# Optimization experiments

Measured on AMD Instinct MI355X. Metric: run time of the kernel, lower is better.

The kernel has to match this reference:

```python
import jax, jax.numpy as jnp
import numpy as np

B, S, D = 8, 2048, 768
SCALE = jnp.sqrt(jnp.float32(D))


def setup_inputs() -> dict:
    key = jax.random.key(0)
    ks = jax.random.split(key, 9)
    sd = 1.0 / np.sqrt(D)
    return {
        "x": jax.random.normal(ks[0], (B, S, D), jnp.float32),
        "Wq": jax.random.normal(ks[1], (D, D), jnp.float32) * sd,
        "bq": jax.random.normal(ks[2], (D,), jnp.float32) * sd,
        "Wk": jax.random.normal(ks[3], (D, D), jnp.float32) * sd,
        "bk": jax.random.normal(ks[4], (D,), jnp.float32) * sd,
        "Wv": jax.random.normal(ks[5], (D, D), jnp.float32) * sd,
        "bv": jax.random.normal(ks[6], (D,), jnp.float32) * sd,
        "Wp": jax.random.normal(ks[7], (D, D), jnp.float32) * sd,
        "bp": jax.random.normal(ks[8], (D,), jnp.float32) * sd,
    }


def reference(x, Wq, bq, Wk, bk, Wv, bv, Wp, bp):
    # Linear layers: y = x @ W^T + b (torch nn.Linear convention)
    Q = jnp.einsum("bsd,ed->bse", x, Wq) + bq
    K = jnp.einsum("bsd,ed->bse", x, Wk) + bk
    V = jnp.einsum("bsd,ed->bse", x, Wv) + bv
    # Full attention matrix (no head split in original module)
    alpha = jnp.einsum("bqd,bkd->bqk", Q, K) / SCALE  # [B,S,S]
    alpha = jax.nn.softmax(alpha, axis=-1)
    # dropout is identity in eval mode
    out = jnp.einsum("bqk,bkd->bqd", alpha, V)
    out = jnp.einsum("bsd,ed->bse", out, Wp) + bp
    return out
```

## Files before the change

### kernel.cpp

```cpp
#include <hip/hip_runtime.h>
#include <stdint.h>


typedef __attribute__((ext_vector_type(8))) short short8;
typedef __attribute__((ext_vector_type(4))) float f32x4;

typedef const __attribute__((address_space(1))) void gvoid_t;
typedef __attribute__((address_space(3))) void lvoid_t;

__device__ __forceinline__ float b2f(unsigned short u) {
  union { unsigned int u; float f; } v;
  v.u = ((unsigned int)u) << 16;
  return v.f;
}
__device__ __forceinline__ unsigned short f2b(float f) {
  union { float f; unsigned int u; } v; v.f = f;
  unsigned int u = v.u;
  return (unsigned short)((u + 0x7fffu + ((u >> 16) & 1u)) >> 16);
}

struct Cvt9 {
  const void* s[9];
  unsigned short* d[9];
  long long n8[9];
  long long total8;
};

__global__ __launch_bounds__(256) void convert_inputs(Cvt9 C) {
  long long g = (long long)blockIdx.x * 256 + threadIdx.x;
  if (g >= C.total8) return;
  int s = 0;
  long long off = g;
  while (off >= C.n8[s]) { off -= C.n8[s]; ++s; }
  const float* sf = (const float*)C.s[s] + off * 8;
  unsigned short* dp = C.d[s] + off * 8;
  float4 a = ((const float4*)sf)[0];
  float4 b = ((const float4*)sf)[1];
  uint4 o;
  o.x = (unsigned int)f2b(a.x) | ((unsigned int)f2b(a.y) << 16);
  o.y = (unsigned int)f2b(a.z) | ((unsigned int)f2b(a.w) << 16);
  o.z = (unsigned int)f2b(b.x) | ((unsigned int)f2b(b.y) << 16);
  o.w = (unsigned int)f2b(b.z) | ((unsigned int)f2b(b.w) << 16);
  *(uint4*)dp = o;
}

template<int NQ>
__device__ __forceinline__ void gemm256(
    const unsigned short* __restrict__ Ag,
    const unsigned short* __restrict__ Bg,
    const int lda, const int ldb, const int NT,
    unsigned short* lds, f32x4 (&acc)[8][NQ])
{
  const int t    = threadIdx.x;
  const int w    = t >> 6;
  const int lane = t & 63;
  const int lo   = lane & 15;
  const int quad = lane >> 4;
  const int wr   = w >> 2;
  const int wcn  = w & 3;
  const int swz  = ((t & 7) ^ ((t >> 3) & 7)) << 3;
  const int wslot = w * 512;
  constexpr int SBUF_B = (4 + NQ) * 8192;
  constexpr int SBUF_S = SBUF_B / 2;

  const unsigned lbase = (unsigned)(uintptr_t)(void*)lds;
  const unsigned sb0 = (unsigned)((quad ^ (lo & 7)) << 4);
  const unsigned sb1 = (unsigned)(((4 + quad) ^ (lo & 7)) << 4);
  const unsigned aA0 = lbase + wr * 16384 + lo * 128 + sb0;
  const unsigned aA1 = lbase + wr * 16384 + lo * 128 + sb1;
  const unsigned bB  = lbase + 32768u + (unsigned)(wcn * 16 * NQ + lo) * 128;
  const unsigned aB0 = bB + sb0;
  const unsigned aB1 = bB + sb1;

  short8 af[4][2], bf0[2][2], bf1[2][2];

#define STG(gb, ld, kt, q, reg)                                                   \
  __builtin_amdgcn_global_load_lds(                                               \
      (gvoid_t*)((gb) + (size_t)((q) * 64 + (t >> 3)) * (ld) + (kt) * 64 + swz),  \
      (lvoid_t*)((reg) + wslot), 16, 0, 0)
#define SA02(kt) { unsigned short* r_ = lds + ((kt) & 1) * SBUF_S;         \
                   STG(Ag, lda, (kt), 0, r_); STG(Ag, lda, (kt), 2, r_ + 8192); }
#define SA13(kt) { unsigned short* r_ = lds + ((kt) & 1) * SBUF_S;         \
                   STG(Ag, lda, (kt), 1, r_ + 4096); STG(Ag, lda, (kt), 3, r_ + 12288); }
#define SBALL(kt) { unsigned short* r_ = lds + ((kt) & 1) * SBUF_S + 16384; \
                    STG(Bg, ldb, (kt), 0, r_); STG(Bg, ldb, (kt), 1, r_ + 4096); \
                    STG(Bg, ldb, (kt), 2, r_ + 8192); \
                    if constexpr (NQ == 4) STG(Bg, ldb, (kt), 3, r_ + 12288); }
#define DSR(d, a, IMM) asm volatile("ds_read_b128 %0, %1 offset:" #IMM : "=v"(d) : "v"(a))
#define RDA(MH, bo) {                                                 \
  const unsigned a0_ = aA0 + (bo) + (MH) * 8192;                      \
  const unsigned a1_ = aA1 + (bo) + (MH) * 8192;                      \
  DSR(af[0][0], a0_, 0);    DSR(af[0][1], a1_, 0);                    \
  DSR(af[1][0], a0_, 2048); DSR(af[1][1], a1_, 2048);                 \
  DSR(af[2][0], a0_, 4096); DSR(af[2][1], a1_, 4096);                 \
  DSR(af[3][0], a0_, 6144); DSR(af[3][1], a1_, 6144); }
#define RDB(BF, NB, NFR, bo) {                                        \
  const unsigned b0_ = aB0 + (bo) + (NB) * 2048;                      \
  const unsigned b1_ = aB1 + (bo) + (NB) * 2048;                      \
  DSR(BF[0][0], b0_, 0);    DSR(BF[0][1], b1_, 0);                    \
  if ((NFR) == 2) { DSR(BF[1][0], b0_, 2048); DSR(BF[1][1], b1_, 2048); } }
#define MMA(MH, NB, BF, NFR) {                                                \
  __builtin_amdgcn_s_barrier();                                               \
  asm volatile("s_waitcnt lgkmcnt(0)" ::: "memory");                          \
  __builtin_amdgcn_sched_barrier(0);                                          \
  __builtin_amdgcn_s_setprio(1);                                              \
  _Pragma("unroll") for (int kc = 0; kc < 2; ++kc)                            \
  _Pragma("unroll") for (int mi = 0; mi < 4; ++mi)                            \
  _Pragma("unroll") for (int ni = 0; ni < (NFR); ++ni)                        \
    acc[(MH)*4 + mi][(NB) + ni] = __builtin_amdgcn_mfma_f32_16x16x32_bf16(    \
        af[mi][kc], BF[ni][kc], acc[(MH)*4 + mi][(NB) + ni], 0, 0, 0);        \
  __builtin_amdgcn_s_setprio(0);                                              \
  __builtin_amdgcn_sched_barrier(0);                                          \
  __builtin_amdgcn_s_barrier(); }
#define VMS() { if constexpr (NQ == 4) asm volatile("s_waitcnt vmcnt(8)" ::: "memory"); \
                else                   asm volatile("s_waitcnt vmcnt(7)" ::: "memory"); }
#define VM0() asm volatile("s_waitcnt vmcnt(0)" ::: "memory")

  SA02(0); SBALL(0); SA13(0);
  SA02(1); SBALL(1); SA13(1);
  VMS();
  __builtin_amdgcn_s_barrier();

  for (int kt = 0; kt < NT - 2; ++kt) {
    const unsigned bo = (unsigned)((kt & 1) * SBUF_B);
    RDA(0, bo); RDB(bf0, 0, 2, bo);                       MMA(0, 0, bf0, 2);
    RDB(bf1, 2, NQ - 2, bo); SA02(kt + 2);                MMA(0, 2, bf1, NQ - 2);
    RDA(1, bo); SBALL(kt + 2);                            MMA(1, 0, bf0, 2);
    SA13(kt + 2); VMS();                                  MMA(1, 2, bf1, NQ - 2);
  }
  {
    const unsigned bo = (unsigned)((NT & 1) * SBUF_B);
    RDA(0, bo); RDB(bf0, 0, 2, bo);                       MMA(0, 0, bf0, 2);
    RDB(bf1, 2, NQ - 2, bo);                              MMA(0, 2, bf1, NQ - 2);
    RDA(1, bo);                                           MMA(1, 0, bf0, 2);
    VM0();                                                MMA(1, 2, bf1, NQ - 2);
  }
  {
    const unsigned bo = (unsigned)(((NT - 1) & 1) * SBUF_B);
    RDA(0, bo); RDB(bf0, 0, 2, bo);                       MMA(0, 0, bf0, 2);
    RDB(bf1, 2, NQ - 2, bo);                              MMA(0, 2, bf1, NQ - 2);
    RDA(1, bo);                                           MMA(1, 0, bf0, 2);
                                                          MMA(1, 2, bf1, NQ - 2);
  }
#undef STG
#undef SA02
#undef SA13
#undef SBALL
#undef DSR
#undef RDA
#undef RDB
#undef MMA
#undef VMS
#undef VM0
}

template<int MODE, int NQ>
__device__ __forceinline__ void epi_bf16(
    unsigned short* Ls, f32x4 (&acc)[8][NQ], int h,
    const unsigned short* bias_n0, const float* rlbase, float scale,
    unsigned short* Cg, int ldc)
{
  constexpr int RS = 64 * NQ + 8;
  const int t = threadIdx.x, w = t >> 6, lane = t & 63;
  const int lo = lane & 15, quad = lane >> 4, wr = w >> 2, wcn = w & 3;
  __syncthreads();
  if (wr == h) {
    float bvv[NQ];
    if (MODE == 0) {
#pragma unroll
      for (int nf = 0; nf < NQ; ++nf) bvv[nf] = b2f(bias_n0[wcn * 16 * NQ + nf * 16 + lo]);
    }
#pragma unroll
    for (int mf = 0; mf < 8; ++mf) {
      const int r0 = mf * 16 + quad * 4;
      float rv[4];
      if (MODE == 3) {
#pragma unroll
        for (int r = 0; r < 4; ++r) rv[r] = __builtin_amdgcn_rcpf(rlbase[h * 128 + r0 + r]);
      }
#pragma unroll
      for (int nf = 0; nf < NQ; ++nf) {
        const int col = wcn * 16 * NQ + nf * 16 + lo;
#pragma unroll
        for (int r = 0; r < 4; ++r) {
          float v = acc[mf][nf][r];
          if (MODE == 0)      v += bvv[nf];
          else if (MODE == 2) v = __expf(fminf(v * scale, 30.f));
          else if (MODE == 3) v *= rv[r];
          Ls[(r0 + r) * RS + col] = f2b(v);
        }
      }
    }
  }
  __syncthreads();
#pragma unroll
  for (int u0 = 0; u0 < 2 * NQ; ++u0) {
    const int u = u0 * 512 + t, row = u / (8 * NQ), c16 = (u % (8 * NQ)) * 8;
    *(uint4*)(Cg + (size_t)(h * 128 + row) * ldc + c16) = *(const uint4*)(Ls + row * RS + c16);
  }
}

__global__ __launch_bounds__(512, 2) void qkv_k(
    const unsigned short* __restrict__ xb,
    const unsigned short* __restrict__ Wq, const unsigned short* __restrict__ bq,
    const unsigned short* __restrict__ Wk, const unsigned short* __restrict__ bk,
    const unsigned short* __restrict__ Wv, const unsigned short* __restrict__ bv,
    unsigned short* __restrict__ qb, unsigned short* __restrict__ kb,
    unsigned short* __restrict__ vt)
{
  __shared__ unsigned short smem[57344];
  const int sel = blockIdx.y >> 2;
  const int n0  = (blockIdx.y & 3) * 192;
  const int m0  = blockIdx.x * 256;

  const unsigned short* W;
  const unsigned short* bi;
  if (sel == 0)      { W = Wq; bi = bq; }
  else if (sel == 1) { W = Wk; bi = bk; }
  else               { W = Wv; bi = bv; }

  f32x4 acc[8][3] = {};
  gemm256<3>(xb + (size_t)m0 * 768, W + (size_t)n0 * 768, 768, 768, 12, smem, acc);

  if (sel < 2) {
    unsigned short* dst = (sel == 0 ? qb : kb) + (size_t)m0 * 768 + n0;
    epi_bf16<0, 3>(smem, acc, 0, bi + n0, nullptr, 0.f, dst, 768);
    epi_bf16<0, 3>(smem, acc, 1, bi + n0, nullptr, 0.f, dst, 768);
    return;
  }

  const int t = threadIdx.x, w = t >> 6, lane = t & 63;
  const int lo = lane & 15, quad = lane >> 4, wr = w >> 2, wcn = w & 3;
  const int bb2 = m0 >> 11, sin = m0 & 2047;
  unsigned short* Ls = smem;
#pragma unroll
  for (int ec = 0; ec < 3; ++ec) {
    __syncthreads();
#pragma unroll
    for (int nf = 0; nf < 3; ++nf) {
      const int ebase = wcn * 48 + nf * 16;
      if ((ebase >> 6) == ec) {
        const float bvv = b2f(bi[n0 + ebase + lo]);
#pragma unroll
        for (int mf = 0; mf < 8; ++mf) {
          const int srow = wr * 128 + mf * 16 + quad * 4;
          ushort4 pk;
          pk.x = f2b(acc[mf][nf][0] + bvv);
          pk.y = f2b(acc[mf][nf][1] + bvv);
          pk.z = f2b(acc[mf][nf][2] + bvv);
          pk.w = f2b(acc[mf][nf][3] + bvv);
          *(ushort4*)(Ls + ((ebase & 63) + lo) * 264 + srow) = pk;
        }
      }
    }
    __syncthreads();
    unsigned short* Vb = vt + (size_t)bb2 * 1572864 + (size_t)(n0 + ec * 64) * 2048 + sin;
#pragma unroll
    for (int u0 = 0; u0 < 4; ++u0) {
      const int u = u0 * 512 + t, e = u >> 5, s16 = (u & 31) * 8;
      *(uint4*)(Vb + (size_t)e * 2048 + s16) = *(const uint4*)(Ls + e * 264 + s16);
    }
  }
}

__global__ __launch_bounds__(512, 2) void score_k(
    const unsigned short* __restrict__ Q, const unsigned short* __restrict__ Kb,
    unsigned short* __restrict__ E, float* __restrict__ rl, float scale)
{
  __shared__ unsigned short smem[65536];
  const int m0 = blockIdx.x * 256, n0 = blockIdx.y * 256, bz = blockIdx.z;

  f32x4 acc[8][4] = {};
  gemm256<4>(Q + (size_t)bz * 1572864 + (size_t)m0 * 768,
             Kb + (size_t)bz * 1572864 + (size_t)n0 * 768, 768, 768, 12, smem, acc);

  const int t = threadIdx.x;
  unsigned short* Eg = E + (size_t)bz * 4194304 + (size_t)m0 * 2048 + n0;
#pragma unroll
  for (int h = 0; h < 2; ++h) {
    epi_bf16<2, 4>(smem, acc, h, nullptr, nullptr, scale, Eg, 2048);
    const int row = t >> 2, seg = t & 3;
    const unsigned short* lr = smem + row * 264 + seg * 64;
    float s = 0.f;
#pragma unroll
    for (int q8 = 0; q8 < 8; ++q8) {
      const int qq = ((q8 + row) & 7) * 8;
      uint4 v = *(const uint4*)(lr + qq);
      unsigned int uu[4] = {v.x, v.y, v.z, v.w};
#pragma unroll
      for (int c = 0; c < 4; ++c)
        s += b2f((unsigned short)(uu[c] & 0xffffu)) + b2f((unsigned short)(uu[c] >> 16));
    }
    s += __shfl_xor(s, 1);
    s += __shfl_xor(s, 2);
    if (seg == 0) atomicAdd(rl + bz * 2048 + m0 + h * 128 + row, s);
  }
}

__global__ __launch_bounds__(512, 2) void pv_k(
    const unsigned short* __restrict__ E, const unsigned short* __restrict__ Vt,
    const float* __restrict__ rl, unsigned short* __restrict__ attn)
{
  __shared__ unsigned short smem[57344];
  const int m0 = blockIdx.x * 256, n0 = blockIdx.y * 192, bz = blockIdx.z;

  f32x4 acc[8][3] = {};
  gemm256<3>(E + (size_t)bz * 4194304 + (size_t)m0 * 2048,
             Vt + (size_t)bz * 1572864 + (size_t)n0 * 2048, 2048, 2048, 32, smem, acc);

  const float* rlb = rl + bz * 2048 + m0;
  unsigned short* Cg = attn + (size_t)bz * 1572864 + (size_t)m0 * 768 + n0;
  epi_bf16<3, 3>(smem, acc, 0, nullptr, rlb, 0.f, Cg, 768);
  epi_bf16<3, 3>(smem, acc, 1, nullptr, rlb, 0.f, Cg, 768);
}

__global__ __launch_bounds__(512, 2) void out_k(
    const unsigned short* __restrict__ attn,
    const unsigned short* __restrict__ Wp, const unsigned short* __restrict__ bp,
    float* __restrict__ Of)
{
  __shared__ unsigned short smem[57344];
  const int m0 = blockIdx.x * 256, n0 = blockIdx.y * 192;

  f32x4 acc[8][3] = {};
  gemm256<3>(attn + (size_t)m0 * 768, Wp + (size_t)n0 * 768, 768, 768, 12, smem, acc);

  const int t = threadIdx.x, w = t >> 6, lane = t & 63;
  const int lo = lane & 15, quad = lane >> 4, wr = w >> 2, wcn = w & 3;
  float* Lf = (float*)smem;
#pragma unroll
  for (int p = 0; p < 4; ++p) {
    __syncthreads();
    if (wr == (p >> 1)) {
#pragma unroll
      for (int mi = 0; mi < 4; ++mi) {
        const int mf = (p & 1) * 4 + mi;
        const int r0 = mi * 16 + quad * 4;
#pragma unroll
        for (int nf = 0; nf < 3; ++nf) {
          const int col = wcn * 48 + nf * 16 + lo;
          const float bvv = b2f(bp[n0 + col]);
#pragma unroll
          for (int r = 0; r < 4; ++r)
            Lf[(r0 + r) * 196 + col] = acc[mf][nf][r] + bvv;
        }
      }
    }
    __syncthreads();
#pragma unroll
    for (int u0 = 0; u0 < 6; ++u0) {
      const int u = u0 * 512 + t, row = u / 48, c4 = (u % 48) * 4;
      *(float4*)(Of + (size_t)(m0 + p * 64 + row) * 768 + n0 + c4) =
          *(const float4*)(Lf + row * 196 + c4);
    }
  }
}

extern "C" void kernel_launch(void* const* d_in, const int* in_sizes, int n_in,
                              void* d_out, int out_size, void* d_ws, size_t ws_size,
                              hipStream_t stream) {
  (void)in_sizes; (void)n_in; (void)out_size; (void)ws_size;

  char* ws = (char*)d_ws;
  float* rl    = (float*)(ws + 4096);
  unsigned short* wcv = (unsigned short*)(ws + ((size_t)1 << 20));
  unsigned short* qb  = (unsigned short*)(ws + ((size_t)8  << 20));
  unsigned short* kb  = (unsigned short*)(ws + ((size_t)32 << 20));
  unsigned short* vt  = (unsigned short*)(ws + ((size_t)56 << 20));
  unsigned short* eb  = (unsigned short*)(ws + ((size_t)80 << 20));
  unsigned short* xb  = eb;
  unsigned short* attn = qb;

  unsigned short* wqb = wcv;
  unsigned short* bqb = wcv + 589824;
  unsigned short* wkb = wcv + 590592;
  unsigned short* bkb = wcv + 1180416;
  unsigned short* wvb = wcv + 1181184;
  unsigned short* bvb = wcv + 1771008;
  unsigned short* wpb = wcv + 1771776;
  unsigned short* bpb = wcv + 2361600;

  const float inv_scale = 0.036084391824351615f;

  Cvt9 cv;
  cv.s[0] = d_in[0]; cv.d[0] = xb;  cv.n8[0] = 12582912 / 8;
  cv.s[1] = d_in[1]; cv.d[1] = wqb; cv.n8[1] = 589824 / 8;
  cv.s[2] = d_in[2]; cv.d[2] = bqb; cv.n8[2] = 768 / 8;
  cv.s[3] = d_in[3]; cv.d[3] = wkb; cv.n8[3] = 589824 / 8;
  cv.s[4] = d_in[4]; cv.d[4] = bkb; cv.n8[4] = 768 / 8;
  cv.s[5] = d_in[5]; cv.d[5] = wvb; cv.n8[5] = 589824 / 8;
  cv.s[6] = d_in[6]; cv.d[6] = bvb; cv.n8[6] = 768 / 8;
  cv.s[7] = d_in[7]; cv.d[7] = wpb; cv.n8[7] = 589824 / 8;
  cv.s[8] = d_in[8]; cv.d[8] = bpb; cv.n8[8] = 768 / 8;
  cv.total8 = (12582912 + 4 * (589824 + 768)) / 8;
  convert_inputs<<<(unsigned)((cv.total8 + 255) / 256), dim3(256), 0, stream>>>(cv);

  hipMemsetAsync(rl, 0, 16384 * sizeof(float), stream);

  qkv_k<<<dim3(64, 12, 1), dim3(512), 0, stream>>>(xb, wqb, bqb, wkb, bkb, wvb, bvb, qb, kb, vt);

  score_k<<<dim3(8, 8, 8), dim3(512), 0, stream>>>(qb, kb, eb, rl, inv_scale);

  pv_k<<<dim3(8, 4, 8), dim3(512), 0, stream>>>(eb, vt, rl, attn);

  out_k<<<dim3(64, 4, 1), dim3(512), 0, stream>>>(attn, wpb, bpb, (float*)d_out);
}
```

Baseline: 321.0 us.

## Halve GEMM M-tile to 128 rows and double grid sizes across all kernels

Replaces the 256-row block GEMM with a 128-row variant that uses fewer accumulators, less LDS and a simplified two-phase MMA pipeline. Grids are doubled in M and launch bounds are raised to four blocks per SM. Epilogues are simplified to a single pass. The aim is more blocks for better CU occupancy and wave coverage on the small grids, at the cost of less operand reuse per block and more global traffic for the B operand.

After: 337.4 us. 1.05x slower.

```diff
diff --git a/kernel.cpp b/kernel.cpp
--- a/kernel.cpp
+++ b/kernel.cpp
@@ -45,11 +45,11 @@
 }
 
 template<int NQ>
-__device__ __forceinline__ void gemm256(
+__device__ __forceinline__ void gemm128(
     const unsigned short* __restrict__ Ag,
     const unsigned short* __restrict__ Bg,
     const int lda, const int ldb, const int NT,
-    unsigned short* lds, f32x4 (&acc)[8][NQ])
+    unsigned short* lds, f32x4 (&acc)[4][NQ])
 {
   const int t    = threadIdx.x;
   const int w    = t >> 6;
@@ -60,103 +60,93 @@
   const int wcn  = w & 3;
   const int swz  = ((t & 7) ^ ((t >> 3) & 7)) << 3;
   const int wslot = w * 512;
-  constexpr int SBUF_B = (4 + NQ) * 8192;
+  constexpr int SBUF_B = (2 + NQ) * 8192;
   constexpr int SBUF_S = SBUF_B / 2;
 
   const unsigned lbase = (unsigned)(uintptr_t)(void*)lds;
   const unsigned sb0 = (unsigned)((quad ^ (lo & 7)) << 4);
   const unsigned sb1 = (unsigned)(((4 + quad) ^ (lo & 7)) << 4);
-  const unsigned aA0 = lbase + wr * 16384 + lo * 128 + sb0;
-  const unsigned aA1 = lbase + wr * 16384 + lo * 128 + sb1;
-  const unsigned bB  = lbase + 32768u + (unsigned)(wcn * 16 * NQ + lo) * 128;
-  const unsigned aB0 = bB + sb0;
-  const unsigned aB1 = bB + sb1;
-
-  short8 af[4][2], bf0[2][2], bf1[2][2];
-
-#define STG(gb, ld, kt, q, reg)                                                   \
+  const unsigned aA0 = lbase + (unsigned)(wr * 64 + lo) * 128 + sb0;
+  const unsigned aA1 = lbase + (unsigned)(wr * 64 + lo) * 128 + sb1;
+  const unsigned aB0 = lbase + 16384u + (unsigned)(wcn * 16 * NQ + lo) * 128 + sb0;
+  const unsigned aB1 = lbase + 16384u + (unsigned)(wcn * 16 * NQ + lo) * 128 + sb1;
+
+  short8 af[4][2], bf[NQ][2];
+
+#define STG(gb, ld, kt, q, soff)                                                  \
   __builtin_amdgcn_global_load_lds(                                               \
       (gvoid_t*)((gb) + (size_t)((q) * 64 + (t >> 3)) * (ld) + (kt) * 64 + swz),  \
-      (lvoid_t*)((reg) + wslot), 16, 0, 0)
-#define SA02(kt) { unsigned short* r_ = lds + ((kt) & 1) * SBUF_S;         \
-                   STG(Ag, lda, (kt), 0, r_); STG(Ag, lda, (kt), 2, r_ + 8192); }
-#define SA13(kt) { unsigned short* r_ = lds + ((kt) & 1) * SBUF_S;         \
-                   STG(Ag, lda, (kt), 1, r_ + 4096); STG(Ag, lda, (kt), 3, r_ + 12288); }
-#define SBALL(kt) { unsigned short* r_ = lds + ((kt) & 1) * SBUF_S + 16384; \
-                    STG(Bg, ldb, (kt), 0, r_); STG(Bg, ldb, (kt), 1, r_ + 4096); \
-                    STG(Bg, ldb, (kt), 2, r_ + 8192); \
-                    if constexpr (NQ == 4) STG(Bg, ldb, (kt), 3, r_ + 12288); }
+      (lvoid_t*)(lds + ((kt) & 1) * SBUF_S + (soff) + wslot), 16, 0, 0)
+#define SALL(kt) { STG(Ag, lda, (kt), 0, 0); STG(Ag, lda, (kt), 1, 4096);      \
+                   STG(Bg, ldb, (kt), 0, 8192); STG(Bg, ldb, (kt), 1, 12288);  \
+                   STG(Bg, ldb, (kt), 2, 16384);                               \
+                   if constexpr (NQ == 4) STG(Bg, ldb, (kt), 3, 20480); }
 #define DSR(d, a, IMM) asm volatile("ds_read_b128 %0, %1 offset:" #IMM : "=v"(d) : "v"(a))
-#define RDA(MH, bo) {                                                 \
-  const unsigned a0_ = aA0 + (bo) + (MH) * 8192;                      \
-  const unsigned a1_ = aA1 + (bo) + (MH) * 8192;                      \
+#define RDALL(bo) {                                                   \
+  const unsigned a0_ = aA0 + (bo);                                    \
+  const unsigned a1_ = aA1 + (bo);                                    \
   DSR(af[0][0], a0_, 0);    DSR(af[0][1], a1_, 0);                    \
   DSR(af[1][0], a0_, 2048); DSR(af[1][1], a1_, 2048);                 \
   DSR(af[2][0], a0_, 4096); DSR(af[2][1], a1_, 4096);                 \
-  DSR(af[3][0], a0_, 6144); DSR(af[3][1], a1_, 6144); }
-#define RDB(BF, NB, NFR, bo) {                                        \
-  const unsigned b0_ = aB0 + (bo) + (NB) * 2048;                      \
-  const unsigned b1_ = aB1 + (bo) + (NB) * 2048;                      \
-  DSR(BF[0][0], b0_, 0);    DSR(BF[0][1], b1_, 0);                    \
-  if ((NFR) == 2) { DSR(BF[1][0], b0_, 2048); DSR(BF[1][1], b1_, 2048); } }
-#define MMA(MH, NB, BF, NFR) {                                                \
+  DSR(af[3][0], a0_, 6144); DSR(af[3][1], a1_, 6144);                 \
+  const unsigned b0_ = aB0 + (bo);                                    \
+  const unsigned b1_ = aB1 + (bo);                                    \
+  DSR(bf[0][0], b0_, 0);    DSR(bf[0][1], b1_, 0);                    \
+  DSR(bf[1][0], b0_, 2048); DSR(bf[1][1], b1_, 2048);                 \
+  DSR(bf[2][0], b0_, 4096); DSR(bf[2][1], b1_, 4096);                 \
+  if constexpr (NQ == 4) { DSR(bf[3][0], b0_, 6144); DSR(bf[3][1], b1_, 6144); } }
+#define MMA(NLO, NHI) {                                                       \
   __builtin_amdgcn_s_barrier();                                               \
   asm volatile("s_waitcnt lgkmcnt(0)" ::: "memory");                          \
   __builtin_amdgcn_sched_barrier(0);                                          \
   __builtin_amdgcn_s_setprio(1);                                              \
   _Pragma("unroll") for (int kc = 0; kc < 2; ++kc)                            \
   _Pragma("unroll") for (int mi = 0; mi < 4; ++mi)                            \
-  _Pragma("unroll") for (int ni = 0; ni < (NFR); ++ni)                        \
-    acc[(MH)*4 + mi][(NB) + ni] = __builtin_amdgcn_mfma_f32_16x16x32_bf16(    \
-        af[mi][kc], BF[ni][kc], acc[(MH)*4 + mi][(NB) + ni], 0, 0, 0);        \
+  _Pragma("unroll") for (int ni = (NLO); ni < (NHI); ++ni)                    \
+    acc[mi][ni] = __builtin_amdgcn_mfma_f32_16x16x32_bf16(                    \
+        af[mi][kc], bf[ni][kc], acc[mi][ni], 0, 0, 0);                        \
   __builtin_amdgcn_s_setprio(0);                                              \
   __builtin_amdgcn_sched_barrier(0);                                          \
   __builtin_amdgcn_s_barrier(); }
-#define VMS() { if constexpr (NQ == 4) asm volatile("s_waitcnt vmcnt(8)" ::: "memory"); \
-                else                   asm volatile("s_waitcnt vmcnt(7)" ::: "memory"); }
-#define VM0() asm volatile("s_waitcnt vmcnt(0)" ::: "memory")
-
-  SA02(0); SBALL(0); SA13(0);
-  SA02(1); SBALL(1); SA13(1);
-  VMS();
+#define VMN() { if constexpr (NQ == 3) asm volatile("s_waitcnt vmcnt(5)" ::: "memory"); \
+                else                   asm volatile("s_waitcnt vmcnt(6)" ::: "memory"); }
+
+  SALL(0); SALL(1);
+  VMN();
   __builtin_amdgcn_s_barrier();
 
   for (int kt = 0; kt < NT - 2; ++kt) {
     const unsigned bo = (unsigned)((kt & 1) * SBUF_B);
-    RDA(0, bo); RDB(bf0, 0, 2, bo);                       MMA(0, 0, bf0, 2);
-    RDB(bf1, 2, NQ - 2, bo); SA02(kt + 2);                MMA(0, 2, bf1, NQ - 2);
-    RDA(1, bo); SBALL(kt + 2);                            MMA(1, 0, bf0, 2);
-    SA13(kt + 2); VMS();                                  MMA(1, 2, bf1, NQ - 2);
+    RDALL(bo);
+    MMA(0, 2);
+    SALL(kt + 2);
+    VMN();
+    MMA(2, NQ);
   }
   {
     const unsigned bo = (unsigned)((NT & 1) * SBUF_B);
-    RDA(0, bo); RDB(bf0, 0, 2, bo);                       MMA(0, 0, bf0, 2);
-    RDB(bf1, 2, NQ - 2, bo);                              MMA(0, 2, bf1, NQ - 2);
-    RDA(1, bo);                                           MMA(1, 0, bf0, 2);
-    VM0();                                                MMA(1, 2, bf1, NQ - 2);
+    RDALL(bo);
+    MMA(0, 2);
+    asm volatile("s_waitcnt vmcnt(0)" ::: "memory");
+    MMA(2, NQ);
   }
   {
     const unsigned bo = (unsigned)(((NT - 1) & 1) * SBUF_B);
-    RDA(0, bo); RDB(bf0, 0, 2, bo);                       MMA(0, 0, bf0, 2);
-    RDB(bf1, 2, NQ - 2, bo);                              MMA(0, 2, bf1, NQ - 2);
-    RDA(1, bo);                                           MMA(1, 0, bf0, 2);
-                                                          MMA(1, 2, bf1, NQ - 2);
+    RDALL(bo);
+    MMA(0, 2);
+    MMA(2, NQ);
   }
 #undef STG
-#undef SA02
-#undef SA13
-#undef SBALL
+#undef SALL
 #undef DSR
-#undef RDA
-#undef RDB
+#undef RDALL
 #undef MMA
-#undef VMS
-#undef VM0
+#undef VMN
 }
 
 template<int MODE, int NQ>
 __device__ __forceinline__ void epi_bf16(
-    unsigned short* Ls, f32x4 (&acc)[8][NQ], int h,
+    unsigned short* Ls, f32x4 (&acc)[4][NQ],
     const unsigned short* bias_n0, const float* rlbase, float scale,
     unsigned short* Cg, int ldc)
 {
@@ -164,19 +154,19 @@
   const int t = threadIdx.x, w = t >> 6, lane = t & 63;
   const int lo = lane & 15, quad = lane >> 4, wr = w >> 2, wcn = w & 3;
   __syncthreads();
-  if (wr == h) {
+  {
     float bvv[NQ];
     if (MODE == 0) {
 #pragma unroll
       for (int nf = 0; nf < NQ; ++nf) bvv[nf] = b2f(bias_n0[wcn * 16 * NQ + nf * 16 + lo]);
     }
 #pragma unroll
-    for (int mf = 0; mf < 8; ++mf) {
-      const int r0 = mf * 16 + quad * 4;
+    for (int mf = 0; mf < 4; ++mf) {
+      const int r0 = wr * 64 + mf * 16 + quad * 4;
       float rv[4];
       if (MODE == 3) {
 #pragma unroll
-        for (int r = 0; r < 4; ++r) rv[r] = __builtin_amdgcn_rcpf(rlbase[h * 128 + r0 + r]);
+        for (int r = 0; r < 4; ++r) rv[r] = __builtin_amdgcn_rcpf(rlbase[r0 + r]);
       }
 #pragma unroll
       for (int nf = 0; nf < NQ; ++nf) {
@@ -196,11 +186,11 @@
 #pragma unroll
   for (int u0 = 0; u0 < 2 * NQ; ++u0) {
     const int u = u0 * 512 + t, row = u / (8 * NQ), c16 = (u % (8 * NQ)) * 8;
-    *(uint4*)(Cg + (size_t)(h * 128 + row) * ldc + c16) = *(const uint4*)(Ls + row * RS + c16);
-  }
-}
-
-__global__ __launch_bounds__(512, 2) void qkv_k(
+    *(uint4*)(Cg + (size_t)row * ldc + c16) = *(const uint4*)(Ls + row * RS + c16);
+  }
+}
+
+__global__ __launch_bounds__(512, 4) void qkv_k(
     const unsigned short* __restrict__ xb,
     const unsigned short* __restrict__ Wq, const unsigned short* __restrict__ bq,
     const unsigned short* __restrict__ Wk, const unsigned short* __restrict__ bk,
@@ -208,10 +198,10 @@
     unsigned short* __restrict__ qb, unsigned short* __restrict__ kb,
     unsigned short* __restrict__ vt)
 {
-  __shared__ unsigned short smem[57344];
+  __shared__ unsigned short smem[40960];
   const int sel = blockIdx.y >> 2;
   const int n0  = (blockIdx.y & 3) * 192;
-  const int m0  = blockIdx.x * 256;
+  const int m0  = blockIdx.x * 128;
 
   const unsigned short* W;
   const unsigned short* bi;
@@ -219,13 +209,12 @@
   else if (sel == 1) { W = Wk; bi = bk; }
   else               { W = Wv; bi = bv; }
 
-  f32x4 acc[8][3] = {};
-  gemm256<3>(xb + (size_t)m0 * 768, W + (size_t)n0 * 768, 768, 768, 12, smem, acc);
+  f32x4 acc[4][3] = {};
+  gemm128<3>(xb + (size_t)m0 * 768, W + (size_t)n0 * 768, 768, 768, 12, smem, acc);
 
   if (sel < 2) {
     unsigned short* dst = (sel == 0 ? qb : kb) + (size_t)m0 * 768 + n0;
-    epi_bf16<0, 3>(smem, acc, 0, bi + n0, nullptr, 0.f, dst, 768);
-    epi_bf16<0, 3>(smem, acc, 1, bi + n0, nullptr, 0.f, dst, 768);
+    epi_bf16<0, 3>(smem, acc, bi + n0, nullptr, 0.f, dst, 768);
     return;
   }
 
@@ -242,23 +231,23 @@
       if ((ebase >> 6) == ec) {
         const float bvv = b2f(bi[n0 + ebase + lo]);
 #pragma unroll
-        for (int mf = 0; mf < 8; ++mf) {
-          const int srow = wr * 128 + mf * 16 + quad * 4;
+        for (int mf = 0; mf < 4; ++mf) {
+          const int srow = wr * 64 + mf * 16 + quad * 4;
           ushort4 pk;
           pk.x = f2b(acc[mf][nf][0] + bvv);
           pk.y = f2b(acc[mf][nf][1] + bvv);
           pk.z = f2b(acc[mf][nf][2] + bvv);
           pk.w = f2b(acc[mf][nf][3] + bvv);
-          *(ushort4*)(Ls + ((ebase & 63) + lo) * 264 + srow) = pk;
+          *(ushort4*)(Ls + ((ebase & 63) + lo) * 136 + srow) = pk;
         }
       }
     }
     __syncthreads();
     unsigned short* Vb = vt + (size_t)bb2 * 1572864 + (size_t)(n0 + ec * 64) * 2048 + sin;
 #pragma unroll
-    for (int u0 = 0; u0 < 4; ++u0) {
-      const int u = u0 * 512 + t, e = u >> 5, s16 = (u & 31) * 8;
-      *(uint4*)(Vb + (size_t)e * 2048 + s16) = *(const uint4*)(Ls + e * 264 + s16);
+    for (int u0 = 0; u0 < 2; ++u0) {
+      const int u = u0 * 512 + t, e = u >> 4, s16 = (u & 15) * 8;
+      *(uint4*)(Vb + (size_t)e * 2048 + s16) = *(const uint4*)(Ls + e * 136 + s16);
     }
   }
 }
@@ -267,82 +256,78 @@
     const unsigned short* __restrict__ Q, const unsigned short* __restrict__ Kb,
     unsigned short* __restrict__ E, float* __restrict__ rl, float scale)
 {
-  __shared__ unsigned short smem[65536];
-  const int m0 = blockIdx.x * 256, n0 = blockIdx.y * 256, bz = blockIdx.z;
-
-  f32x4 acc[8][4] = {};
-  gemm256<4>(Q + (size_t)bz * 1572864 + (size_t)m0 * 768,
+  __shared__ unsigned short smem[49152];
+  const int m0 = blockIdx.x * 128, n0 = blockIdx.y * 256, bz = blockIdx.z;
+
+  f32x4 acc[4][4] = {};
+  gemm128<4>(Q + (size_t)bz * 1572864 + (size_t)m0 * 768,
              Kb + (size_t)bz * 1572864 + (size_t)n0 * 768, 768, 768, 12, smem, acc);
 
+  unsigned short* Eg = E + (size_t)bz * 4194304 + (size_t)m0 * 2048 + n0;
+  epi_bf16<2, 4>(smem, acc, nullptr, nullptr, scale, Eg, 2048);
+
   const int t = threadIdx.x;
-  unsigned short* Eg = E + (size_t)bz * 4194304 + (size_t)m0 * 2048 + n0;
-#pragma unroll
-  for (int h = 0; h < 2; ++h) {
-    epi_bf16<2, 4>(smem, acc, h, nullptr, nullptr, scale, Eg, 2048);
-    const int row = t >> 2, seg = t & 3;
-    const unsigned short* lr = smem + row * 264 + seg * 64;
-    float s = 0.f;
-#pragma unroll
-    for (int q8 = 0; q8 < 8; ++q8) {
-      const int qq = ((q8 + row) & 7) * 8;
-      uint4 v = *(const uint4*)(lr + qq);
-      unsigned int uu[4] = {v.x, v.y, v.z, v.w};
-#pragma unroll
-      for (int c = 0; c < 4; ++c)
-        s += b2f((unsigned short)(uu[c] & 0xffffu)) + b2f((unsigned short)(uu[c] >> 16));
-    }
-    s += __shfl_xor(s, 1);
-    s += __shfl_xor(s, 2);
-    if (seg == 0) atomicAdd(rl + bz * 2048 + m0 + h * 128 + row, s);
-  }
-}
-
-__global__ __launch_bounds__(512, 2) void pv_k(
+  const int row = t >> 2, seg = t & 3;
+  const unsigned short* lr = smem + row * 264 + seg * 64;
+  float s = 0.f;
+#pragma unroll
+  for (int q8 = 0; q8 < 8; ++q8) {
+    const int qq = ((q8 + row) & 7) * 8;
+    uint4 v = *(const uint4*)(lr + qq);
+    unsigned int uu[4] = {v.x, v.y, v.z, v.w};
+#pragma unroll
+    for (int c = 0; c < 4; ++c)
+      s += b2f((unsigned short)(uu[c] & 0xffffu)) + b2f((unsigned short)(uu[c] >> 16));
+  }
+  s += __shfl_xor(s, 1);
+  s += __shfl_xor(s, 2);
+  if (seg == 0) atomicAdd(rl + bz * 2048 + m0 + row, s);
+}
+
+__global__ __launch_bounds__(512, 4) void pv_k(
     const unsigned short* __restrict__ E, const unsigned short* __restrict__ Vt,
     const float* __restrict__ rl, unsigned short* __restrict__ attn)
 {
-  __shared__ unsigned short smem[57344];
-  const int m0 = blockIdx.x * 256, n0 = blockIdx.y * 192, bz = blockIdx.z;
-
-  f32x4 acc[8][3] = {};
-  gemm256<3>(E + (size_t)bz * 4194304 + (size_t)m0 * 2048,
+  __shared__ unsigned short smem[40960];
+  const int m0 = blockIdx.x * 128, n0 = blockIdx.y * 192, bz = blockIdx.z;
+
+  f32x4 acc[4][3] = {};
+  gemm128<3>(E + (size_t)bz * 4194304 + (size_t)m0 * 2048,
              Vt + (size_t)bz * 1572864 + (size_t)n0 * 2048, 2048, 2048, 32, smem, acc);
 
   const float* rlb = rl + bz * 2048 + m0;
   unsigned short* Cg = attn + (size_t)bz * 1572864 + (size_t)m0 * 768 + n0;
-  epi_bf16<3, 3>(smem, acc, 0, nullptr, rlb, 0.f, Cg, 768);
-  epi_bf16<3, 3>(smem, acc, 1, nullptr, rlb, 0.f, Cg, 768);
-}
-
-__global__ __launch_bounds__(512, 2) void out_k(
+  epi_bf16<3, 3>(smem, acc, nullptr, rlb, 0.f, Cg, 768);
+}
+
+__global__ __launch_bounds__(512, 4) void out_k(
     const unsigned short* __restrict__ attn,
     const unsigned short* __restrict__ Wp, const unsigned short* __restrict__ bp,
     float* __restrict__ Of)
 {
-  __shared__ unsigned short smem[57344];
-  const int m0 = blockIdx.x * 256, n0 = blockIdx.y * 192;
-
-  f32x4 acc[8][3] = {};
-  gemm256<3>(attn + (size_t)m0 * 768, Wp + (size_t)n0 * 768, 768, 768, 12, smem, acc);
+  __shared__ unsigned short smem[40960];
+  const int m0 = blockIdx.x * 128, n0 = blockIdx.y * 192;
+
+  f32x4 acc[4][3] = {};
+  gemm128<3>(attn + (size_t)m0 * 768, Wp + (size_t)n0 * 768, 768, 768, 12, smem, acc);
 
   const int t = threadIdx.x, w = t >> 6, lane = t & 63;
   const int lo = lane & 15, quad = lane >> 4, wr = w >> 2, wcn = w & 3;
   float* Lf = (float*)smem;
 #pragma unroll
-  for (int p = 0; p < 4; ++p) {
+  for (int p = 0; p < 2; ++p) {
     __syncthreads();
-    if (wr == (p >> 1)) {
-#pragma unroll
-      for (int mi = 0; mi < 4; ++mi) {
-        const int mf = (p & 1) * 4 + mi;
-        const int r0 = mi * 16 + quad * 4;
+    if (wr == p) {
+#pragma unroll
+      for (int mf = 0; mf < 4; ++mf) {
+        const int r0 = mf * 16 + quad * 4;
 #pragma unroll
         for (int nf = 0; nf < 3; ++nf) {
           const int col = wcn * 48 + nf * 16 + lo;
           const float bvv = b2f(bp[n0 + col]);
 #pragma unroll
           for (int r = 0; r < 4; ++r)
-            Lf[(r0 + r) * 196 + col] = acc[mf][nf][r] + bvv;
+            Lf[(r0 + r) * 200 + col] = acc[mf][nf][r] + bvv;
         }
       }
     }
@@ -351,7 +336,7 @@
     for (int u0 = 0; u0 < 6; ++u0) {
       const int u = u0 * 512 + t, row = u / 48, c4 = (u % 48) * 4;
       *(float4*)(Of + (size_t)(m0 + p * 64 + row) * 768 + n0 + c4) =
-          *(const float4*)(Lf + row * 196 + c4);
+          *(const float4*)(Lf + row * 200 + c4);
     }
   }
 }
@@ -397,11 +382,11 @@
 
   hipMemsetAsync(rl, 0, 16384 * sizeof(float), stream);
 
-  qkv_k<<<dim3(64, 12, 1), dim3(512), 0, stream>>>(xb, wqb, bqb, wkb, bkb, wvb, bvb, qb, kb, vt);
-
-  score_k<<<dim3(8, 8, 8), dim3(512), 0, stream>>>(qb, kb, eb, rl, inv_scale);
-
-  pv_k<<<dim3(8, 4, 8), dim3(512), 0, stream>>>(eb, vt, rl, attn);
-
-  out_k<<<dim3(64, 4, 1), dim3(512), 0, stream>>>(attn, wpb, bpb, (float*)d_out);
-}
+  qkv_k<<<dim3(128, 12, 1), dim3(512), 0, stream>>>(xb, wqb, bqb, wkb, bkb, wvb, bvb, qb, kb, vt);
+
+  score_k<<<dim3(16, 8, 8), dim3(512), 0, stream>>>(qb, kb, eb, rl, inv_scale);
+
+  pv_k<<<dim3(16, 4, 8), dim3(512), 0, stream>>>(eb, vt, rl, attn);
+
+  out_k<<<dim3(128, 4, 1), dim3(512), 0, stream>>>(attn, wpb, bpb, (float*)d_out);
+}
```
